# Performance work log

Measured on AMD Instinct MI355X. Metric: run time of the kernel, lower is better.

Reference implementation:

```python
import jax, jax.numpy as jnp
import numpy as np
import math

SPATIAL_SHAPES = ((128, 128), (64, 64), (32, 32), (16, 16))
D_MODEL, N_HEADS, N_LEVELS, N_POINTS = 256, 8, 4, 4
D_HEAD = D_MODEL // N_HEADS


def grid_sample_bilinear(value, grid):
    """F.grid_sample(mode='bilinear', padding_mode='zeros', align_corners=False).
    value: (B, D, H, W); grid: (B, Q, K, 2) with coords in ~[-1, 1] (x, y order).
    Returns (B, D, Q, K)."""
    B, D, H, W = value.shape
    Q, K = grid.shape[1], grid.shape[2]
    x = (grid[..., 0] + 1.0) * (W * 0.5) - 0.5  # pixel-space x
    y = (grid[..., 1] + 1.0) * (H * 0.5) - 0.5
    x0 = jnp.floor(x)
    y0 = jnp.floor(y)
    wx = x - x0
    wy = y - y0
    x0i = x0.astype(jnp.int32)
    y0i = y0.astype(jnp.int32)
    vf = value.reshape(B, D, H * W)

    def corner(xi, yi, w):
        valid = (xi >= 0) & (xi < W) & (yi >= 0) & (yi < H)
        idx = jnp.clip(yi, 0, H - 1) * W + jnp.clip(xi, 0, W - 1)  # (B,Q,K)
        v = jax.vmap(lambda t, i: t[:, i])(vf, idx.reshape(B, Q * K))  # (B,D,Q*K)
        return v * (w * valid.astype(w.dtype)).reshape(B, 1, Q * K)

    out = (corner(x0i, y0i, (1 - wx) * (1 - wy))
           + corner(x0i + 1, y0i, wx * (1 - wy))
           + corner(x0i, y0i + 1, (1 - wx) * wy)
           + corner(x0i + 1, y0i + 1, wx * wy))
    return out.reshape(B, D, Q, K)


def _offset_bias():
    # torch _reset_parameters: rotational grid init for sampling_offsets bias
    thetas = jnp.arange(N_HEADS, dtype=jnp.float32) * (2.0 * math.pi / N_HEADS)
    g = jnp.stack([jnp.cos(thetas), jnp.sin(thetas)], -1)  # (M,2)
    g = g / jnp.max(jnp.abs(g), axis=-1, keepdims=True)
    g = jnp.tile(g[:, None, None, :], (1, N_LEVELS, N_POINTS, 1))  # (M,L,P,2)
    g = g * (jnp.arange(N_POINTS, dtype=jnp.float32) % 4 + 1)[None, None, :, None]
    return g.reshape(-1)


def setup_inputs() -> dict:
    key = jax.random.key(0)
    ks = jax.random.split(key, 10)
    N = 2
    Lq = sum(h * w for h, w in SPATIAL_SHAPES)  # 21760
    inp = {
        'query': jax.random.normal(ks[0], (N, Lq, D_MODEL), jnp.float32),
        'reference_points': jax.random.uniform(ks[1], (N, Lq, N_LEVELS, 1, 2), jnp.float32),
    }
    for l, (H, W) in enumerate(SPATIAL_SHAPES):
        inp[f'value{l}'] = jax.random.normal(ks[2 + l], (N * N_HEADS, D_HEAD, H * W), jnp.float32)
    inp['W_off'] = jax.random.normal(ks[6], (D_MODEL, N_HEADS * N_LEVELS * N_POINTS * 2), jnp.float32) * 0.02
    inp['b_off'] = _offset_bias()
    inp['W_attn'] = jax.random.normal(ks[7], (D_MODEL, N_HEADS * N_LEVELS * N_POINTS), jnp.float32) * 0.02
    inp['b_attn'] = jax.random.normal(ks[8], (N_HEADS * N_LEVELS * N_POINTS,), jnp.float32) * 0.02
    return inp


def reference(query, reference_points, value0, value1, value2, value3, W_off, b_off, W_attn, b_attn):
    N, Lq, _ = query.shape
    M, L, P, D = N_HEADS, N_LEVELS, N_POINTS, D_HEAD
    # linear projections
    off = (query @ W_off + b_off).reshape(N, Lq, M, L, P, 2)
    attn = jax.nn.softmax((query @ W_attn + b_attn).reshape(N, Lq, M, L * P), axis=-1)
    attn = attn.reshape(N, Lq, M, L, P)
    # reference_points: (N, A, L, G, 2) -> transpose(2,3) -> flatten(1,2) -> (N, Lq, L, 2)
    ref = jnp.transpose(reference_points, (0, 1, 3, 2, 4)).reshape(N, Lq, L, 2)
    norm = jnp.array([[w, h] for (h, w) in SPATIAL_SHAPES], jnp.float32)  # flipped: (W,H) per level
    loc = ref[:, :, None, :, None, :] + off / norm[None, None, None, :, None, :]  # (N,Lq,M,L,P,2)
    grids = jnp.transpose(2.0 * loc - 1.0, (0, 2, 1, 3, 4, 5)).reshape(N * M, Lq, L, P, 2)
    values = (value0, value1, value2, value3)
    samples = []
    for l, (H, W) in enumerate(SPATIAL_SHAPES):
        v = values[l].reshape(N * M, D, H, W)
        samples.append(grid_sample_bilinear(v, grids[:, :, l]))  # (N*M, D, Lq, P)
    samp = jnp.concatenate(samples, axis=-1)  # (N*M, D, Lq, L*P)
    aw = jnp.transpose(attn, (0, 2, 1, 3, 4)).reshape(N * M, 1, Lq, L * P)
    out = (samp * aw).sum(-1).reshape(N, M * D, Lq)
    return jnp.transpose(out, (0, 2, 1))  # (N, Lq, C)
```

## Files before the change

kernel.cpp:

```cpp
#include <hip/hip_runtime.h>
#include <hip/hip_fp16.h>
#include <math.h>

#define NB     2
#define LQ     21760
#define NQTOT  (NB * LQ)
#define DM     256
#define NH     8
#define DH     32
#define NL     4
#define NP     4

typedef __attribute__((ext_vector_type(8))) short    bf16x8;
typedef __attribute__((ext_vector_type(4))) float    f32x4;
typedef __attribute__((ext_vector_type(8))) unsigned short ushort8;

__device__ __forceinline__ unsigned short f2bf(float x) {
  union { float f; unsigned int u; } c; c.f = x;
  const unsigned int lsb = (c.u >> 16) & 1u;
  c.u += 0x7fffu + lsb;
  return (unsigned short)(c.u >> 16);
}

__global__ __launch_bounds__(256) void msda_transpose(
    const float* __restrict__ in, __half* __restrict__ out, int HW) {
  __shared__ float tile[32][33];
  const int nm   = blockIdx.y;
  const int pos0 = blockIdx.x * 32;
  const int tx = threadIdx.x & 31;
  const int ty = threadIdx.x >> 5;
  const float* ip = in + (size_t)nm * 32 * HW;
  __half2* op = reinterpret_cast<__half2*>(out + (size_t)nm * HW * 32);
#pragma unroll
  for (int i = 0; i < 4; i++) {
    const int d = ty + i * 8;
    tile[d][tx] = ip[(size_t)d * HW + pos0 + tx];
  }
  __syncthreads();
  const int h  = threadIdx.x & 15;
  const int r0 = threadIdx.x >> 4;
#pragma unroll
  for (int i = 0; i < 2; i++) {
    const int r = r0 + i * 16;
    op[(size_t)(pos0 + r) * 16 + h] =
        __floats2half2_rn(tile[2 * h][r], tile[2 * h + 1][r]);
  }
}

__global__ __launch_bounds__(256) void msda_cast_w(
    const float* __restrict__ W_off, const float* __restrict__ W_attn,
    unsigned short* __restrict__ Wt) {
  __shared__ float tile[32][33];
  const int n0 = blockIdx.x * 32;
  const int k0 = blockIdx.y * 32;
  const int tx = threadIdx.x & 31;
  const int ty = threadIdx.x >> 5;
#pragma unroll
  for (int i = 0; i < 4; i++) {
    const int k = k0 + ty + i * 8;
    const int n = n0 + tx;
    const float v = (blockIdx.x < 8) ? W_off[(size_t)k * 256 + n]
                                     : W_attn[(size_t)k * 128 + (n - 256)];
    tile[ty + i * 8][tx] = v;
  }
  __syncthreads();
#pragma unroll
  for (int i = 0; i < 4; i++) {
    const int nl = ty + i * 8;
    Wt[(size_t)(n0 + nl) * 256 + k0 + tx] = f2bf(tile[tx][nl]);
  }
}

__global__ __launch_bounds__(256) void msda_gemm16(
    const float* __restrict__ Q, const unsigned short* __restrict__ Wt,
    const float* __restrict__ b_off, const float* __restrict__ b_attn,
    float* __restrict__ Cout) {
  __shared__ unsigned short sA[128 * 64];
  __shared__ unsigned short sB[128 * 64];

  const int t    = threadIdx.x;
  const int lane = t & 63;
  const int wid  = t >> 6;
  const int m0   = blockIdx.x * 128;
  const int n0   = blockIdx.y * 128;
  const int wm   = wid >> 1, wn = wid & 1;

  const int sr = t >> 3;
  const int sc = t & 7;

  f32x4 acc[4][4] = {};

  for (int ck = 0; ck < 4; ++ck) {
    const int k0 = ck * 64;
#pragma unroll
    for (int i = 0; i < 4; ++i) {
      const int m = i * 32 + sr;
      const float* src = Q + (size_t)(m0 + m) * DM + k0 + sc * 8;
      const float4 a0 = *reinterpret_cast<const float4*>(src);
      const float4 a1 = *reinterpret_cast<const float4*>(src + 4);
      ushort8 v;
      v[0] = f2bf(a0.x); v[1] = f2bf(a0.y); v[2] = f2bf(a0.z); v[3] = f2bf(a0.w);
      v[4] = f2bf(a1.x); v[5] = f2bf(a1.y); v[6] = f2bf(a1.z); v[7] = f2bf(a1.w);
      const int byte = m * 128 + ((sc * 16) ^ ((m & 7) << 4));
      *reinterpret_cast<ushort8*>(reinterpret_cast<char*>(sA) + byte) = v;
    }
#pragma unroll
    for (int i = 0; i < 4; ++i) {
      const int nr = i * 32 + sr;
      const ushort8 b = *reinterpret_cast<const ushort8*>(
          Wt + (size_t)(n0 + nr) * 256 + k0 + sc * 8);
      const int byte = nr * 128 + ((sc * 16) ^ ((nr & 7) << 4));
      *reinterpret_cast<ushort8*>(reinterpret_cast<char*>(sB) + byte) = b;
    }
    __syncthreads();
#pragma unroll
    for (int ks = 0; ks < 2; ++ks) {
      bf16x8 af[4], bfr[4];
#pragma unroll
      for (int f = 0; f < 4; ++f) {
        const int ar = wm * 64 + f * 16 + (lane & 15);
        const int ab = ar * 128 + ((ks * 64 + (lane >> 4) * 16) ^ ((ar & 7) << 4));
        af[f] = *reinterpret_cast<const bf16x8*>(
            reinterpret_cast<const char*>(sA) + ab);
        const int br = wn * 64 + f * 16 + (lane & 15);
        const int bb = br * 128 + ((ks * 64 + (lane >> 4) * 16) ^ ((br & 7) << 4));
        bfr[f] = *reinterpret_cast<const bf16x8*>(
            reinterpret_cast<const char*>(sB) + bb);
      }
#pragma unroll
      for (int mi = 0; mi < 4; ++mi)
#pragma unroll
        for (int ni = 0; ni < 4; ++ni)
          acc[mi][ni] = __builtin_amdgcn_mfma_f32_16x16x32_bf16(
              af[mi], bfr[ni], acc[mi][ni], 0, 0, 0);
    }
    __syncthreads();
  }

#pragma unroll
  for (int ni = 0; ni < 4; ++ni) {
    const int col = n0 + wn * 64 + ni * 16 + (lane & 15);
    const float bias = (col < 256) ? b_off[col] : b_attn[col - 256];
#pragma unroll
    for (int mi = 0; mi < 4; ++mi) {
      const int row0 = m0 + wm * 64 + mi * 16 + (lane >> 4) * 4;
#pragma unroll
      for (int r = 0; r < 4; ++r)
        Cout[(size_t)(row0 + r) * 384 + col] = acc[mi][ni][r] + bias;
    }
  }
}

__global__ __launch_bounds__(256, 3) void msda_sample(
    const __half* __restrict__ vt, const float* __restrict__ logits,
    const float* __restrict__ rp, float* __restrict__ out) {
  __shared__ float Ld[4][384];
  __shared__ float Ew[4][128];
  __shared__ float Aw[4][128];
  __shared__ float Rf[4][8];
  __shared__ float Op[4][NH][36];

  const int t = threadIdx.x;
  const int w = t >> 6;
  const int u = t & 63;
  const int n = blockIdx.y;
  const int q = blockIdx.x * 4 + w;
  const int qi = n * LQ + q;

  const float* lg = logits + (size_t)qi * 384;
  for (int i = u; i < 384; i += 64) Ld[w][i] = lg[i];
  if (u < 8) Rf[w][u] = rp[(size_t)qi * 8 + u];
  __syncthreads();

#pragma unroll
  for (int r = 0; r < 4; r++) {
    const int j = u + 64 * r;
    const int m = j >> 5, rest = j & 31;
    const int l = rest >> 3, pc = rest & 7;
    Op[w][m][l * 9 + pc] = Ld[w][j];
  }
#pragma unroll
  for (int r = 0; r < 2; r++) {
    const int j = u + 64 * r;
    const int h4 = j & ~15;
    float mx = -1e30f;
#pragma unroll
    for (int i = 0; i < 16; i++) mx = fmaxf(mx, Ld[w][256 + h4 + i]);
    Ew[w][j] = __expf(Ld[w][256 + j] - mx);
  }
  __syncthreads();
#pragma unroll
  for (int r = 0; r < 2; r++) {
    const int j = u + 64 * r;
    const int h4 = j & ~15;
    float den = 0.f;
#pragma unroll
    for (int i = 0; i < 16; i++) den += Ew[w][h4 + i];
    Aw[w][j] = Ew[w][j] / den;
  }
  __syncthreads();

  const int m = u >> 3;
  const int d0 = (u & 7) * 4;
  float4 acc; acc.x = acc.y = acc.z = acc.w = 0.f;

  const size_t LB[4] = {0, 8388608, 10485760, 11010048};
#pragma unroll
  for (int l = 0; l < 4; l++) {
    const int Wl = 128 >> l;
    const int HW = Wl * Wl;
    const __half* vp = vt + LB[l] + ((size_t)(n * NH + m) * HW) * DH + d0;

    const float fx = fmaf(Rf[w][2 * l + 0], (float)Wl, -0.5f);
    const float fy = fmaf(Rf[w][2 * l + 1], (float)Wl, -0.5f);

    uint2  cv[4][4];
    float  cw[4][4];
#pragma unroll
    for (int p = 0; p < 4; p++) {
      const float ox = Op[w][m][l * 9 + 2 * p + 0];
      const float oy = Op[w][m][l * 9 + 2 * p + 1];
      const float aw = Aw[w][m * 16 + l * 4 + p];
      const float xp = fx + ox;
      const float yp = fy + oy;
      const float x0f = floorf(xp), y0f = floorf(yp);
      const float wx = xp - x0f, wy = yp - y0f;
      const int x0 = (int)x0f, y0 = (int)y0f;
      const int x1 = x0 + 1,   y1 = y0 + 1;
      const float vx0 = ((unsigned)x0 < (unsigned)Wl) ? 1.f : 0.f;
      const float vx1 = ((unsigned)x1 < (unsigned)Wl) ? 1.f : 0.f;
      const float vy0 = ((unsigned)y0 < (unsigned)Wl) ? 1.f : 0.f;
      const float vy1 = ((unsigned)y1 < (unsigned)Wl) ? 1.f : 0.f;
      const int x0c = min(max(x0, 0), Wl - 1), x1c = min(max(x1, 0), Wl - 1);
      const int y0c = min(max(y0, 0), Wl - 1), y1c = min(max(y1, 0), Wl - 1);

      cw[p][0] = aw * (1.f - wx) * (1.f - wy) * vx0 * vy0;
      cw[p][1] = aw * wx * (1.f - wy) * vx1 * vy0;
      cw[p][2] = aw * (1.f - wx) * wy * vx0 * vy1;
      cw[p][3] = aw * wx * wy * vx1 * vy1;

      cv[p][0] = *reinterpret_cast<const uint2*>(vp + (y0c * Wl + x0c) * DH);
      cv[p][1] = *reinterpret_cast<const uint2*>(vp + (y0c * Wl + x1c) * DH);
      cv[p][2] = *reinterpret_cast<const uint2*>(vp + (y1c * Wl + x0c) * DH);
      cv[p][3] = *reinterpret_cast<const uint2*>(vp + (y1c * Wl + x1c) * DH);
    }
#pragma unroll
    for (int p = 0; p < 4; p++)
#pragma unroll
      for (int c = 0; c < 4; c++) {
        union { uint2 ui; __half2 h[2]; } cvt;
        cvt.ui = cv[p][c];
        const float2 lo = __half22float2(cvt.h[0]);
        const float2 hi = __half22float2(cvt.h[1]);
        const float wgt = cw[p][c];
        acc.x = fmaf(lo.x, wgt, acc.x);
        acc.y = fmaf(lo.y, wgt, acc.y);
        acc.z = fmaf(hi.x, wgt, acc.z);
        acc.w = fmaf(hi.y, wgt, acc.w);
      }
  }
  *reinterpret_cast<float4*>(out + (size_t)qi * DM + u * 4) = acc;
}

extern "C" void kernel_launch(void* const* d_in, const int* in_sizes, int n_in,
                              void* d_out, int out_size, void* d_ws, size_t ws_size,
                              hipStream_t stream) {
  const float* query  = (const float*)d_in[0];
  const float* rp     = (const float*)d_in[1];
  const float* val[4] = {(const float*)d_in[2], (const float*)d_in[3],
                         (const float*)d_in[4], (const float*)d_in[5]};
  const float* W_off  = (const float*)d_in[6];
  const float* b_off  = (const float*)d_in[7];
  const float* W_attn = (const float*)d_in[8];
  const float* b_attn = (const float*)d_in[9];
  float* out = (float*)d_out;

  __half* vt16  = (__half*)d_ws;
  float* logits = (float*)((char*)d_ws + 11141120ull * sizeof(__half));
  unsigned short* Wt = (unsigned short*)((char*)d_ws +
      11141120ull * sizeof(__half) + 16711680ull * sizeof(float));

  const int HWs[4]   = {16384, 4096, 1024, 256};
  const size_t LB[4] = {0, 8388608, 10485760, 11010048};
  for (int l = 0; l < 4; l++) {
    dim3 g(HWs[l] / 32, 16);
    msda_transpose<<<g, 256, 0, stream>>>(val[l], vt16 + LB[l], HWs[l]);
  }

  msda_cast_w<<<dim3(12, 8), 256, 0, stream>>>(W_off, W_attn, Wt);

  msda_gemm16<<<dim3(NQTOT / 128, 3), 256, 0, stream>>>(
      query, Wt, b_off, b_attn, logits);

  msda_sample<<<dim3(LQ / 4, NB), 256, 0, stream>>>(vt16, logits, rp, out);
}
```

Measured before the change: 282.7 us.

## Merge value transposes into one kernel and precompute bilinear weights per sample

Replaces the four per-level transpose launches with a single kernel. It uses 256-position tiles, float4 loads into XOR-swizzled LDS, and 16-byte fp16 stores, which cuts launch count and improves load/store vectorization. In the sampling kernel, each (head, level, point) bilinear weight and corner offset is now computed once into shared memory instead of redundantly by all 8 lanes of a head. This adds LDS footprint (about 17 KB) and another barrier, which may lower occupancy at launch bound 3.

Result: no change. 280.7 us (-0.7%).

```diff
diff --git a/kernel.cpp b/kernel.cpp
--- a/kernel.cpp
+++ b/kernel.cpp
@@ -22,28 +22,58 @@
   return (unsigned short)(c.u >> 16);
 }
 
-__global__ __launch_bounds__(256) void msda_transpose(
-    const float* __restrict__ in, __half* __restrict__ out, int HW) {
-  __shared__ float tile[32][33];
-  const int nm   = blockIdx.y;
-  const int pos0 = blockIdx.x * 32;
-  const int tx = threadIdx.x & 31;
-  const int ty = threadIdx.x >> 5;
-  const float* ip = in + (size_t)nm * 32 * HW;
-  __half2* op = reinterpret_cast<__half2*>(out + (size_t)nm * HW * 32);
-#pragma unroll
-  for (int i = 0; i < 4; i++) {
-    const int d = ty + i * 8;
-    tile[d][tx] = ip[(size_t)d * HW + pos0 + tx];
-  }
-  __syncthreads();
-  const int h  = threadIdx.x & 15;
-  const int r0 = threadIdx.x >> 4;
-#pragma unroll
-  for (int i = 0; i < 2; i++) {
-    const int r = r0 + i * 16;
-    op[(size_t)(pos0 + r) * 16 + h] =
-        __floats2half2_rn(tile[2 * h][r], tile[2 * h + 1][r]);
+__global__ __launch_bounds__(256) void msda_transpose_all(
+    const float* __restrict__ v0, const float* __restrict__ v1,
+    const float* __restrict__ v2, const float* __restrict__ v3,
+    __half* __restrict__ out) {
+  __shared__ float ls[32 * 256];
+  char* lsb = reinterpret_cast<char*>(ls);
+
+  const int t   = threadIdx.x;
+  const int bid = blockIdx.x;
+  const int nm  = bid / 85;
+  const int r   = bid % 85;
+  int l, base;
+  if (r < 64)      { l = 0; base = 0;  }
+  else if (r < 80) { l = 1; base = 64; }
+  else if (r < 84) { l = 2; base = 80; }
+  else             { l = 3; base = 84; }
+  const int HW   = 16384 >> (2 * l);
+  const int pos0 = (r - base) * 256;
+  const float* vsrc = (l == 0) ? v0 : (l == 1) ? v1 : (l == 2) ? v2 : v3;
+  const size_t LBl  = (l == 0) ? 0ull : (l == 1) ? 8388608ull
+                     : (l == 2) ? 10485760ull : 11010048ull;
+
+  const int ch = t >> 3;
+  const int c8 = t & 7;
+  const float* ip = vsrc + (size_t)nm * 32 * HW + pos0;
+#pragma unroll
+  for (int i = 0; i < 8; i++) {
+    const int chunk = c8 + 8 * i;
+    const float4 a = *reinterpret_cast<const float4*>(
+        ip + (size_t)ch * HW + chunk * 4);
+    const int byte = ch * 1024 + ((chunk * 16) ^ ((ch & 7) << 4));
+    *reinterpret_cast<float4*>(lsb + byte) = a;
+  }
+  __syncthreads();
+
+  __half2 o[16];
+#pragma unroll
+  for (int c2 = 0; c2 < 16; c2++) {
+    const int ca = 2 * c2, cb = 2 * c2 + 1;
+    const float va = *reinterpret_cast<const float*>(
+        lsb + ca * 1024 + ((t * 4) ^ ((ca & 7) << 4)));
+    const float vb = *reinterpret_cast<const float*>(
+        lsb + cb * 1024 + ((t * 4) ^ ((cb & 7) << 4)));
+    o[c2] = __floats2half2_rn(va, vb);
+  }
+  __half* op = out + LBl + ((size_t)nm * HW + pos0 + t) * 32;
+#pragma unroll
+  for (int k = 0; k < 4; k++) {
+    union { __half2 h[4]; float4 f; } pk;
+    pk.h[0] = o[4 * k + 0]; pk.h[1] = o[4 * k + 1];
+    pk.h[2] = o[4 * k + 2]; pk.h[3] = o[4 * k + 3];
+    *reinterpret_cast<float4*>(op + k * 8) = pk.f;
   }
 }
 
@@ -159,6 +189,8 @@
   __shared__ float Aw[4][128];
   __shared__ float Rf[4][8];
   __shared__ float Op[4][NH][36];
+  __shared__ float4 Wt4[4][136];
+  __shared__ int4   Of4[4][136];
 
   const int t = threadIdx.x;
   const int w = t >> 6;
@@ -200,6 +232,44 @@
   }
   __syncthreads();
 
+#pragma unroll
+  for (int r = 0; r < 2; r++) {
+    const int j  = u + 64 * r;
+    const int m  = j >> 4;
+    const int lp = j & 15;
+    const int l  = lp >> 2;
+    const int p  = j & 3;
+    const int sh = 7 - l;
+    const int Wl = 1 << sh;
+    const float fx = fmaf(Rf[w][2 * l + 0], (float)Wl, -0.5f);
+    const float fy = fmaf(Rf[w][2 * l + 1], (float)Wl, -0.5f);
+    const float ox = Op[w][m][l * 9 + 2 * p + 0];
+    const float oy = Op[w][m][l * 9 + 2 * p + 1];
+    const float aw = Aw[w][j];
+    const float xp = fx + ox;
+    const float yp = fy + oy;
+    const float x0f = floorf(xp), y0f = floorf(yp);
+    const float wx = xp - x0f, wy = yp - y0f;
+    const int x0 = (int)x0f, y0 = (int)y0f;
+    const int x1 = x0 + 1,   y1 = y0 + 1;
+    const float vx0 = ((unsigned)x0 < (unsigned)Wl) ? 1.f : 0.f;
+    const float vx1 = ((unsigned)x1 < (unsigned)Wl) ? 1.f : 0.f;
+    const float vy0 = ((unsigned)y0 < (unsigned)Wl) ? 1.f : 0.f;
+    const float vy1 = ((unsigned)y1 < (unsigned)Wl) ? 1.f : 0.f;
+    const int x0c = min(max(x0, 0), Wl - 1), x1c = min(max(x1, 0), Wl - 1);
+    const int y0c = min(max(y0, 0), Wl - 1), y1c = min(max(y1, 0), Wl - 1);
+    const int idx = m * 17 + lp;
+    Wt4[w][idx] = make_float4(aw * (1.f - wx) * (1.f - wy) * vx0 * vy0,
+                              aw * wx * (1.f - wy) * vx1 * vy0,
+                              aw * (1.f - wx) * wy * vx0 * vy1,
+                              aw * wx * wy * vx1 * vy1);
+    Of4[w][idx] = make_int4(((y0c << sh) + x0c) << 5,
+                            ((y0c << sh) + x1c) << 5,
+                            ((y1c << sh) + x0c) << 5,
+                            ((y1c << sh) + x1c) << 5);
+  }
+  __syncthreads();
+
   const int m = u >> 3;
   const int d0 = (u & 7) * 4;
   float4 acc; acc.x = acc.y = acc.z = acc.w = 0.f;
@@ -207,57 +277,37 @@
   const size_t LB[4] = {0, 8388608, 10485760, 11010048};
 #pragma unroll
   for (int l = 0; l < 4; l++) {
-    const int Wl = 128 >> l;
-    const int HW = Wl * Wl;
+    const int HW = (128 >> l) * (128 >> l);
     const __half* vp = vt + LB[l] + ((size_t)(n * NH + m) * HW) * DH + d0;
 
-    const float fx = fmaf(Rf[w][2 * l + 0], (float)Wl, -0.5f);
-    const float fy = fmaf(Rf[w][2 * l + 1], (float)Wl, -0.5f);
-
     uint2  cv[4][4];
-    float  cw[4][4];
+    float4 w4[4];
 #pragma unroll
     for (int p = 0; p < 4; p++) {
-      const float ox = Op[w][m][l * 9 + 2 * p + 0];
-      const float oy = Op[w][m][l * 9 + 2 * p + 1];
-      const float aw = Aw[w][m * 16 + l * 4 + p];
-      const float xp = fx + ox;
-      const float yp = fy + oy;
-      const float x0f = floorf(xp), y0f = floorf(yp);
-      const float wx = xp - x0f, wy = yp - y0f;
-      const int x0 = (int)x0f, y0 = (int)y0f;
-      const int x1 = x0 + 1,   y1 = y0 + 1;
-      const float vx0 = ((unsigned)x0 < (unsigned)Wl) ? 1.f : 0.f;
-      const float vx1 = ((unsigned)x1 < (unsigned)Wl) ? 1.f : 0.f;
-      const float vy0 = ((unsigned)y0 < (unsigned)Wl) ? 1.f : 0.f;
-      const float vy1 = ((unsigned)y1 < (unsigned)Wl) ? 1.f : 0.f;
-      const int x0c = min(max(x0, 0), Wl - 1), x1c = min(max(x1, 0), Wl - 1);
-      const int y0c = min(max(y0, 0), Wl - 1), y1c = min(max(y1, 0), Wl - 1);
-
-      cw[p][0] = aw * (1.f - wx) * (1.f - wy) * vx0 * vy0;
-      cw[p][1] = aw * wx * (1.f - wy) * vx1 * vy0;
-      cw[p][2] = aw * (1.f - wx) * wy * vx0 * vy1;
-      cw[p][3] = aw * wx * wy * vx1 * vy1;
-
-      cv[p][0] = *reinterpret_cast<const uint2*>(vp + (y0c * Wl + x0c) * DH);
-      cv[p][1] = *reinterpret_cast<const uint2*>(vp + (y0c * Wl + x1c) * DH);
-      cv[p][2] = *reinterpret_cast<const uint2*>(vp + (y1c * Wl + x0c) * DH);
-      cv[p][3] = *reinterpret_cast<const uint2*>(vp + (y1c * Wl + x1c) * DH);
-    }
-#pragma unroll
-    for (int p = 0; p < 4; p++)
+      const int idx = m * 17 + l * 4 + p;
+      w4[p] = Wt4[w][idx];
+      const int4 o4 = Of4[w][idx];
+      cv[p][0] = *reinterpret_cast<const uint2*>(vp + o4.x);
+      cv[p][1] = *reinterpret_cast<const uint2*>(vp + o4.y);
+      cv[p][2] = *reinterpret_cast<const uint2*>(vp + o4.z);
+      cv[p][3] = *reinterpret_cast<const uint2*>(vp + o4.w);
+    }
+#pragma unroll
+    for (int p = 0; p < 4; p++) {
+      const float cw[4] = {w4[p].x, w4[p].y, w4[p].z, w4[p].w};
 #pragma unroll
       for (int c = 0; c < 4; c++) {
         union { uint2 ui; __half2 h[2]; } cvt;
         cvt.ui = cv[p][c];
         const float2 lo = __half22float2(cvt.h[0]);
         const float2 hi = __half22float2(cvt.h[1]);
-        const float wgt = cw[p][c];
+        const float wgt = cw[c];
         acc.x = fmaf(lo.x, wgt, acc.x);
         acc.y = fmaf(lo.y, wgt, acc.y);
         acc.z = fmaf(hi.x, wgt, acc.z);
         acc.w = fmaf(hi.y, wgt, acc.w);
       }
+    }
   }
   *reinterpret_cast<float4*>(out + (size_t)qi * DM + u * 4) = acc;
 }
@@ -267,8 +317,6 @@
                               hipStream_t stream) {
   const float* query  = (const float*)d_in[0];
   const float* rp     = (const float*)d_in[1];
-  const float* val[4] = {(const float*)d_in[2], (const float*)d_in[3],
-                         (const float*)d_in[4], (const float*)d_in[5]};
   const float* W_off  = (const float*)d_in[6];
   const float* b_off  = (const float*)d_in[7];
   const float* W_attn = (const float*)d_in[8];
@@ -280,12 +328,9 @@
   unsigned short* Wt = (unsigned short*)((char*)d_ws +
       11141120ull * sizeof(__half) + 16711680ull * sizeof(float));
 
-  const int HWs[4]   = {16384, 4096, 1024, 256};
-  const size_t LB[4] = {0, 8388608, 10485760, 11010048};
-  for (int l = 0; l < 4; l++) {
-    dim3 g(HWs[l] / 32, 16);
-    msda_transpose<<<g, 256, 0, stream>>>(val[l], vt16 + LB[l], HWs[l]);
-  }
+  msda_transpose_all<<<dim3(85 * 16), 256, 0, stream>>>(
+      (const float*)d_in[2], (const float*)d_in[3],
+      (const float*)d_in[4], (const float*)d_in[5], vt16);
 
   msda_cast_w<<<dim3(12, 8), 256, 0, stream>>>(W_off, W_attn, Wt);
 
```
